# Kernel optimization log

Measured on AMD Instinct MI355X. Metric: run time of the kernel, lower is better.

The kernel has to match this reference:

```python
import jax, jax.numpy as jnp
import numpy as np
from jax import lax

# ---- constants matching init kwargs / proposal_creator(mode='testing') ----
RATIOS = (0.5, 1.0, 2.0)
SCALES = (8.0, 16.0, 32.0)
BASE = 16.0          # generate_anchor_base base_size
STRIDE = 16          # feat_stride
NMS_THRESH = 0.7
N_PRE = 3000         # n_test_pre_nms
N_POST = 300         # n_test_post_nms
MIN_SIZE = 16.0      # min_size * scale (scale=1)


def _anchor_base():
    # (9, 4) xyxy anchors centered at (BASE/2, BASE/2); ratios outer, scales inner
    r = np.array(RATIOS, np.float32)
    s = np.array(SCALES, np.float32)
    hs = (BASE * s[None, :] * np.sqrt(r)[:, None]).reshape(-1)
    ws = (BASE * s[None, :] * np.sqrt(1.0 / r)[:, None]).reshape(-1)
    cx = cy = BASE / 2.0
    return np.stack([cx - ws / 2, cy - hs / 2, cx + ws / 2, cy + hs / 2], 1).astype(np.float32)


def _all_anchors(h, w):
    # _enumerate_shifted_anchor: shift grid flattened y-outer/x-inner to match
    # permute(0,2,3,1).view(n,-1,4) layout of the conv outputs.
    base = jnp.asarray(_anchor_base())                     # (9,4)
    sx = jnp.arange(w, dtype=jnp.float32) * STRIDE
    sy = jnp.arange(h, dtype=jnp.float32) * STRIDE
    SX, SY = jnp.meshgrid(sx, sy)                          # (h,w)
    shifts = jnp.stack([SX, SY, SX, SY], -1).reshape(-1, 4)  # (h*w,4)
    return (shifts[:, None, :] + base[None, :, :]).reshape(-1, 4)  # (h*w*9,4)


def _proposals(loc, score, anchor, img_h, img_w):
    # loc: (K,4) deltas, score: (K,) fg prob, anchor: (K,4) xyxy
    aw = anchor[:, 2] - anchor[:, 0]
    ah = anchor[:, 3] - anchor[:, 1]
    acx = anchor[:, 0] + 0.5 * aw
    acy = anchor[:, 1] + 0.5 * ah
    cx = loc[:, 0] * aw + acx
    cy = loc[:, 1] * ah + acy
    bw = aw * jnp.exp(loc[:, 2])
    bh = ah * jnp.exp(loc[:, 3])
    x1 = jnp.clip(cx - 0.5 * bw, 0.0, img_w)
    y1 = jnp.clip(cy - 0.5 * bh, 0.0, img_h)
    x2 = jnp.clip(cx + 0.5 * bw, 0.0, img_w)
    y2 = jnp.clip(cy + 0.5 * bh, 0.0, img_h)
    boxes = jnp.stack([x1, y1, x2, y2], 1)
    valid = ((x2 - x1) >= MIN_SIZE) & ((y2 - y1) >= MIN_SIZE)
    # min-size filter -> sink invalid boxes with -inf score, then top-k pre-NMS
    masked = jnp.where(valid, score, -jnp.inf)
    _, idx = lax.top_k(masked, N_PRE)
    b = boxes[idx]                                         # (N_PRE,4), score-sorted desc
    v = valid[idx]
    # pairwise IoU (torchvision convention: no +1)
    area = (b[:, 2] - b[:, 0]) * (b[:, 3] - b[:, 1])
    ix1 = jnp.maximum(b[:, None, 0], b[None, :, 0])
    iy1 = jnp.maximum(b[:, None, 1], b[None, :, 1])
    ix2 = jnp.minimum(b[:, None, 2], b[None, :, 2])
    iy2 = jnp.minimum(b[:, None, 3], b[None, :, 3])
    inter = jnp.clip(ix2 - ix1, 0.0) * jnp.clip(iy2 - iy1, 0.0)
    union = area[:, None] + area[None, :] - inter
    iou = jnp.where(union > 0.0, inter / union, 0.0)
    sup = iou > NMS_THRESH                                 # (N_PRE,N_PRE) bool
    # greedy sequential NMS over score order
    ar = jnp.arange(N_PRE)
    def body(keep, i):
        keep = keep & ~(keep[i] & sup[i] & (ar > i))
        return keep, None
    keep, _ = lax.scan(body, v, ar)
    # first N_POST kept boxes (score order); pad by cycling kept boxes
    order = jnp.argsort(jnp.where(keep, ar, N_PRE))        # kept indices first, sorted
    nk = jnp.maximum(keep.sum(), 1)
    pos = jnp.arange(N_POST)
    sel = order[jnp.where(pos < nk, pos, pos % nk)]
    return b[sel]                                          # (N_POST,4)


def setup_inputs() -> dict:
    key = jax.random.key(0)
    ks = jax.random.split(key, 4)
    n, c, h, w = 4, 512, 38, 38
    return {
        "x": jax.random.normal(ks[0], (n, c, h, w), jnp.float32),
        "conv1_w": jax.random.normal(ks[1], (512, 512, 3, 3), jnp.float32) * 0.01,
        "conv1_b": jnp.zeros((512,), jnp.float32),
        "score_w": jax.random.normal(ks[2], (18, 512), jnp.float32) * 0.01,
        "score_b": jnp.zeros((18,), jnp.float32),
        "loc_w": jax.random.normal(ks[3], (36, 512), jnp.float32) * 0.01,
        "loc_b": jnp.zeros((36,), jnp.float32),
        "img_h": 608,
        "img_w": 608,
    }


def reference(x, conv1_w, conv1_b, score_w, score_b, loc_w, loc_b, img_h, img_w):
    n, _, h, w = x.shape
    feat = jax.nn.relu(
        lax.conv_general_dilated(x, conv1_w, (1, 1), "SAME",
                                 dimension_numbers=("NCHW", "OIHW", "NCHW"))
        + conv1_b[None, :, None, None])
    locs = jnp.einsum("nchw,oc->nohw", feat, loc_w) + loc_b[None, :, None, None]
    scores = jnp.einsum("nchw,oc->nohw", feat, score_w) + score_b[None, :, None, None]
    rpn_locs = locs.transpose(0, 2, 3, 1).reshape(n, -1, 4)      # (n, h*w*9, 4)
    rpn_scores = scores.transpose(0, 2, 3, 1).reshape(n, -1, 2)  # (n, h*w*9, 2)
    fg = jax.nn.softmax(rpn_scores, axis=-1)[..., 1]             # (n, h*w*9)
    anchor = _all_anchors(h, w)
    ih = jnp.float32(img_h)
    iw = jnp.float32(img_w)
    rois = jax.vmap(lambda l, s: _proposals(l, s, anchor, ih, iw))(rpn_locs, fg)
    rois_indices = jnp.broadcast_to(
        jnp.arange(n, dtype=x.dtype)[:, None], (n, N_POST))
    return rpn_locs, rpn_scores, rois.reshape(-1, 4), rois_indices, anchor[None]
```

## Files before the change

kernel.cpp:

```cpp
#include <hip/hip_runtime.h>
#include <cstdint>
#include <cstddef>

#define HW    1444
#define NA    12996
#define NPRE  3000
#define NW    47
#define NPOST 300

#define OFF_LOCS   0
#define OFF_SCORES 207936
#define OFF_ROIS   311904
#define OFF_IDX    316704
#define OFF_ANCH   317904

#define INVALID_KEY 0xFFF0000000000000ULL

typedef float f32x2 __attribute__((ext_vector_type(2)));
typedef float f32x4 __attribute__((ext_vector_type(4)));

__device__ inline double as_dim(int raw) {
  if (raw > 0 && raw < 1000000) return (double)raw;
  return (double)__int_as_float(raw);
}

__global__ __launch_bounds__(256) void wt_k(const float* __restrict__ lw,
                                            const float* __restrict__ sw,
                                            float* __restrict__ Wt,
                                            unsigned long long* __restrict__ keys) {
  int t = blockIdx.x * 256 + threadIdx.x;
  if (t < 4 * (16384 - NA)) {
    int n2 = t / (16384 - NA), r = t - n2 * (16384 - NA);
    keys[((size_t)n2 << 14) + NA + r] = ~0ULL;
  }
  if (t >= 64 * 512) return;
  int o = t & 63, c = t >> 6;
  float v = 0.f;
  if (o < 36)      v = lw[o * 512 + c];
  else if (o < 54) v = sw[(o - 36) * 512 + c];
  Wt[t] = v;
}

__global__ __launch_bounds__(256) void conv_k(const float* __restrict__ X,
                                              const float* __restrict__ W,
                                              const float* __restrict__ B,
                                              float* __restrict__ F) {
  __shared__ float Xs[1008];
  __shared__ float Wsf[2304];
  const int tid  = threadIdx.x;
  const int lane = tid & 63;
  const int wv   = tid >> 6;
  const int seg  = wv * 10;
  const int y  = blockIdx.x;
  const int o0 = blockIdx.y * 64;
  const int n  = blockIdx.z;
  const float* xn = X + ((size_t)n * 512) * HW;

  int xsrcA[2]; bool xvalA[2]; bool xactA1;
  {
    int e = tid;
    int cl = e / 120, rem = e - cl * 120, row = rem / 40, colA = rem - row * 40;
    int m = colA - 1, iy = y - 1 + row;
    xvalA[0] = (m >= 0 && m < 38 && iy >= 0 && iy < 38);
    xsrcA[0] = xvalA[0] ? (cl * HW + iy * 38 + m) : 0;
  }
  {
    int e = tid + 256; xactA1 = (e < 480);
    int cl = e / 120, rem = e - cl * 120, row = rem / 40, colA = rem - row * 40;
    int m = colA - 1, iy = y - 1 + row;
    xvalA[1] = xactA1 && (m >= 0 && m < 38 && iy >= 0 && iy < 38);
    xsrcA[1] = xvalA[1] ? (cl * HW + iy * 38 + m) : 0;
  }
  int xsrcB[3]; bool xvalB[3]; bool xactB2;
#pragma unroll
  for (int u = 0; u < 3; ++u) {
    int e = tid + u * 256;
    bool act = (e < 528);
    int cl = e / 132, rem = e - cl * 132, row = rem / 44, colB = rem - row * 44;
    int m = colB - 3, iy = y - 1 + row;
    xvalB[u] = act && (m >= 0 && m < 38 && iy >= 0 && iy < 38);
    xsrcB[u] = xvalB[u] ? (cl * HW + iy * 38 + m) : 0;
    if (u == 2) xactB2 = act;
  }
  int wsrc[9];
#pragma unroll
  for (int u = 0; u < 9; ++u) {
    int e = tid + u * 256;
    int ol = e / 36, t36 = e - ol * 36;
    wsrc[u] = (o0 + ol) * 4608 + t36;
  }

  float xrA[2], xrB[3], wr_[9];
#pragma unroll
  for (int u = 0; u < 2; ++u) xrA[u] = xvalA[u] ? xn[xsrcA[u]] : 0.f;
#pragma unroll
  for (int u = 0; u < 3; ++u) xrB[u] = xvalB[u] ? xn[xsrcB[u]] : 0.f;
#pragma unroll
  for (int u = 0; u < 9; ++u) wr_[u] = W[wsrc[u]];

  double acc[10];
#pragma unroll
  for (int p = 0; p < 10; ++p) acc[p] = 0.;
  f32x2 pA[5], pB[5];
  float pc0 = 0.f;

  const int  xb0   = (wv & 1) ? (480 + seg + 2) : seg;
  const int  cstep = (wv & 1) ? 132 : 120;
  const int  kstep = (wv & 1) ? 44 : 40;

#define WQ_ELEM(t) ((t & 3) == 0 ? wq[(t) >> 2].x : (t & 3) == 1 ? wq[(t) >> 2].y : \
                    (t & 3) == 2 ? wq[(t) >> 2].z : wq[(t) >> 2].w)

  for (int cc = 0; cc < 128; ++cc) {
    __syncthreads();
    Xs[tid] = xrA[0];
    if (xactA1) Xs[tid + 256] = xrA[1];
    Xs[480 + tid] = xrB[0];
    Xs[480 + tid + 256] = xrB[1];
    if (xactB2) Xs[480 + tid + 512] = xrB[2];
#pragma unroll
    for (int u = 0; u < 9; ++u) Wsf[tid + u * 256] = wr_[u];
    __syncthreads();
    if (cc < 127) {
      const int cb = (cc + 1) * 4;
#pragma unroll
      for (int u = 0; u < 2; ++u) xrA[u] = xvalA[u] ? xn[cb * HW + xsrcA[u]] : 0.f;
#pragma unroll
      for (int u = 0; u < 3; ++u) xrB[u] = xvalB[u] ? xn[cb * HW + xsrcB[u]] : 0.f;
#pragma unroll
      for (int u = 0; u < 9; ++u) wr_[u] = W[wsrc[u] + (cc + 1) * 36];
    }
    f32x4 wq[9];
    {
      const f32x4* wrow = (const f32x4*)&Wsf[lane * 36];
#pragma unroll
      for (int q = 0; q < 9; ++q) wq[q] = wrow[q];
    }
    if ((cc & 1) == 0) {
#pragma unroll
      for (int a = 0; a < 5; ++a) { pA[a] = (f32x2)(0.f); pB[a] = (f32x2)(0.f); }
      pc0 = 0.f;
    }
#pragma unroll
    for (int cl = 0; cl < 4; ++cl) {
      f32x2 wp[9];
#pragma unroll
      for (int k = 0; k < 9; ++k) {
        float wv0 = WQ_ELEM(cl * 9 + k);
        wp[k][0] = wv0; wp[k][1] = wv0;
      }
#pragma unroll
      for (int ky = 0; ky < 3; ++ky) {
        const float* xrow = &Xs[xb0 + cl * cstep + ky * kstep];
        f32x4 q0 = *(const f32x4*)(xrow);
        f32x4 q1 = *(const f32x4*)(xrow + 4);
        f32x4 q2 = *(const f32x4*)(xrow + 8);
        f32x2 xp[6];
        xp[0] = __builtin_shufflevector(q0, q0, 0, 1);
        xp[1] = __builtin_shufflevector(q0, q0, 2, 3);
        xp[2] = __builtin_shufflevector(q1, q1, 0, 1);
        xp[3] = __builtin_shufflevector(q1, q1, 2, 3);
        xp[4] = __builtin_shufflevector(q2, q2, 0, 1);
        xp[5] = __builtin_shufflevector(q2, q2, 2, 3);
#pragma unroll
        for (int a = 0; a < 5; ++a)
          asm("v_pk_fma_f32 %0, %1, %2, %0"
              : "+v"(pA[a]) : "v"(xp[a]), "v"(wp[ky * 3 + 0]));
        pc0 = fmaf(wp[ky * 3 + 1][0], xp[0][1], pc0);
#pragma unroll
        for (int a = 0; a < 5; ++a)
          asm("v_pk_fma_f32 %0, %1, %2, %0"
              : "+v"(pB[a]) : "v"(xp[a + 1]), "v"(wp[ky * 3 + 1]));
#pragma unroll
        for (int a = 0; a < 5; ++a)
          asm("v_pk_fma_f32 %0, %1, %2, %0"
              : "+v"(pA[a]) : "v"(xp[a + 1]), "v"(wp[ky * 3 + 2]));
      }
    }
    if (cc & 1) {
      acc[0] += (double)(pA[0][0] + pc0);
#pragma unroll
      for (int p = 1; p < 10; ++p) {
        float sa = pA[p >> 1][p & 1];
        float sb = (p & 1) ? pB[(p - 1) >> 1][0] : pB[(p - 2) >> 1][1];
        acc[p] += (double)(sa + sb);
      }
    }
  }
  double bb = (double)B[o0 + lane];
  float* fp = F + ((size_t)(n * 512 + o0 + lane)) * HW + y * 38;
#pragma unroll
  for (int p = 0; p < 10; ++p) {
    int col = seg + p;
    if (col < 38) fp[col] = (float)fmax(acc[p] + bb, 0.0);
  }
}

__global__ __launch_bounds__(256) void heads_k(const float* __restrict__ F,
                                               const float* __restrict__ Wt,
                                               const float* __restrict__ lb,
                                               const float* __restrict__ sb,
                                               const int* __restrict__ ihp,
                                               const int* __restrict__ iwp,
                                               float* __restrict__ out,
                                               double* __restrict__ boxes,
                                               unsigned long long* __restrict__ keys) {
  __shared__ float sf[512 * 4];
  __shared__ double ssc[4][18];
  __shared__ float sloc[4][36];
  int n = blockIdx.y;
  int p0 = blockIdx.x * 4;
  int tid = threadIdx.x;
  const float* fn = F + ((size_t)n * 512) * HW;
  for (int e = tid; e < 2048; e += 256) {
    int c = e >> 2, pl = e & 3;
    sf[e] = fn[c * HW + p0 + pl];
  }
  __syncthreads();
  int pl = tid & 3, o = tid >> 2;
  double acc = 0.;
  if (o < 54) {
    for (int c = 0; c < 512; ++c)
      acc = fma((double)Wt[(c << 6) | o], (double)sf[(c << 2) | pl], acc);
  }
  int p = p0 + pl;
  if (o < 36) {
    acc += (double)lb[o];
    float v = (float)acc;
    out[OFF_LOCS + ((size_t)n * NA + (size_t)p * 9 + (o >> 2)) * 4 + (o & 3)] = v;
    sloc[pl][o] = v;
  } else if (o < 54) {
    int oo = o - 36;
    acc += (double)sb[oo];
    out[OFF_SCORES + ((size_t)n * NA + (size_t)p * 9 + (oo >> 1)) * 2 + (oo & 1)] = (float)acc;
    ssc[pl][oo] = acc;
  }
  __syncthreads();
  if (tid < 36) {
    int pl2 = tid / 9, a = tid - pl2 * 9;
    double s0 = ssc[pl2][a * 2], s1 = ssc[pl2][a * 2 + 1];
    double mx = fmax(s0, s1);
    double e0 = exp(s0 - mx), e1 = exp(s1 - mx);
    double sc = e1 / (e0 + e1);
    int pp = p0 + pl2;
    int i = pp * 9 + a;
    int ri = a / 3, si = a - ri * 3;
    double sr  = (ri == 0) ? 0.7071067811865476 : (ri == 1 ? 1.0 : 1.4142135623730951);
    double sri = (ri == 0) ? 1.4142135623730951 : (ri == 1 ? 1.0 : 0.7071067811865476);
    double hs = (double)(128 << si) * sr;
    double wd = (double)(128 << si) * sri;
    int py = pp / 38, px = pp - py * 38;
    float sx = (float)(px * 16), sy = (float)(py * 16);
    float fx1 = (float)(8.0 - 0.5 * wd), fy1 = (float)(8.0 - 0.5 * hs);
    float fx2 = (float)(8.0 + 0.5 * wd), fy2 = (float)(8.0 + 0.5 * hs);
    float ax1f = sx + fx1, ay1f = sy + fy1, ax2f = sx + fx2, ay2f = sy + fy2;
    if (n == 0) {
      float* ap = out + OFF_ANCH + (size_t)i * 4;
      ap[0] = ax1f; ap[1] = ay1f; ap[2] = ax2f; ap[3] = ay2f;
    }
    double ax1 = ax1f, ay1 = ay1f, ax2 = ax2f, ay2 = ay2f;
    double aw = ax2 - ax1, ah = ay2 - ay1;
    double acx = ax1 + 0.5 * aw, acy = ay1 + 0.5 * ah;
    double l0 = (double)sloc[pl2][a * 4 + 0], l1 = (double)sloc[pl2][a * 4 + 1];
    double l2 = (double)sloc[pl2][a * 4 + 2], l3 = (double)sloc[pl2][a * 4 + 3];
    double cx = l0 * aw + acx, cy = l1 * ah + acy;
    double bw = aw * exp(l2), bh = ah * exp(l3);
    double iwf = as_dim(iwp[0]), ihf = as_dim(ihp[0]);
    double x1 = fmin(fmax(cx - 0.5 * bw, 0.0), iwf);
    double y1 = fmin(fmax(cy - 0.5 * bh, 0.0), ihf);
    double x2 = fmin(fmax(cx + 0.5 * bw, 0.0), iwf);
    double y2 = fmin(fmax(cy + 0.5 * bh, 0.0), ihf);
    bool valid = ((x2 - x1) >= 16.0) && ((y2 - y1) >= 16.0);
    double* bp = boxes + ((size_t)n * NA + i) * 4;
    bp[0] = x1; bp[1] = y1; bp[2] = x2; bp[3] = y2;
    unsigned long long u = (unsigned long long)__double_as_longlong(sc);
    u = (u >> 63) ? ~u : (u | 0x8000000000000000ULL);
    unsigned long long inv = ~u;
    if (!valid) inv = INVALID_KEY;
    keys[((size_t)n << 14) + i] = (inv & ~0x3FFFULL) | (unsigned long long)i;
  }
}

__global__ __launch_bounds__(1024) void sortA_k(unsigned long long* __restrict__ keys) {
  __shared__ unsigned long long s[8192];
  const int half = blockIdx.x & 1;
  unsigned long long* g = keys + (((size_t)(blockIdx.x >> 1)) << 14) + ((size_t)half << 13);
  const int tid = threadIdx.x;
  for (int i = tid; i < 8192; i += 1024) s[i] = g[i];
  for (int size = 2; size <= 8192; size <<= 1) {
    for (int stride = size >> 1; stride > 0; stride >>= 1) {
      __syncthreads();
      for (int u = tid; u < 4096; u += 1024) {
        int lo = u & (stride - 1);
        int i1 = ((u - lo) << 1) | lo;
        int i2 = i1 + stride;
        bool up = (i1 & size) == 0;
        if (half) up = !up;
        unsigned long long a = s[i1], b = s[i2];
        if ((a > b) == up) { s[i1] = b; s[i2] = a; }
      }
    }
  }
  __syncthreads();
  for (int i = tid; i < 8192; i += 1024) g[i] = s[i];
}

__global__ __launch_bounds__(1024) void sortCG_k(const unsigned long long* __restrict__ keys,
                                                 const double* __restrict__ boxes,
                                                 double* __restrict__ bsort,
                                                 unsigned long long* __restrict__ vw) {
  __shared__ unsigned long long s[8192];
  const int n = blockIdx.x;
  const unsigned long long* g = keys + ((size_t)n << 14);
  const int tid = threadIdx.x;
  for (int i = tid; i < 8192; i += 1024) {
    unsigned long long a = g[i], b = g[i + 8192];
    s[i] = a < b ? a : b;
  }
  for (int stride = 4096; stride > 0; stride >>= 1) {
    __syncthreads();
    for (int u = tid; u < 4096; u += 1024) {
      int lo = u & (stride - 1);
      int i1 = ((u - lo) << 1) | lo;
      int i2 = i1 + stride;
      unsigned long long a = s[i1], b = s[i2];
      if (a > b) { s[i1] = b; s[i2] = a; }
    }
  }
  __syncthreads();
  const int lane = tid & 63;
#pragma unroll
  for (int r3 = 0; r3 < 3; ++r3) {
    int r = r3 * 1024 + tid;
    bool valid = false;
    if (r < NPRE) {
      unsigned long long kk = s[r];
      valid = kk < INVALID_KEY;
      unsigned idx = (unsigned)(kk & 0x3FFFULL);
      const double* bp = boxes + ((size_t)n * NA + idx) * 4;
      double* dp = bsort + ((size_t)n * NPRE + r) * 4;
      dp[0] = bp[0]; dp[1] = bp[1]; dp[2] = bp[2]; dp[3] = bp[3];
    }
    unsigned long long mask = __ballot(valid);
    int w = r >> 6;
    if (lane == 0 && w < NW) vw[n * NW + w] = mask;
  }
}

__global__ __launch_bounds__(256) void iou_k(const double* __restrict__ bsort,
                                             unsigned long long* __restrict__ sup) {
  int t = blockIdx.x * 256 + threadIdx.x;
  if (t >= 4 * NPRE * NW) return;
  int w = t % NW; int rest = t / NW; int i = rest % NPRE; int n = rest / NPRE;
  const double* bb = bsort + (size_t)n * NPRE * 4;
  double bix1 = bb[(size_t)i*4], biy1 = bb[(size_t)i*4+1];
  double bix2 = bb[(size_t)i*4+2], biy2 = bb[(size_t)i*4+3];
  double ai = (bix2 - bix1) * (biy2 - biy1);
  unsigned long long word = 0ULL;
  int j0 = w << 6;
  if (j0 + 63 > i) {
    int lmax = NPRE - j0; if (lmax > 64) lmax = 64;
    for (int l = 0; l < lmax; ++l) {
      int j = j0 + l;
      if (j <= i) continue;
      const double* bj = bb + (size_t)j * 4;
      double aj = (bj[2] - bj[0]) * (bj[3] - bj[1]);
      double xx1 = fmax(bix1, bj[0]), yy1 = fmax(biy1, bj[1]);
      double xx2 = fmin(bix2, bj[2]), yy2 = fmin(biy2, bj[3]);
      double inter = fmax(xx2 - xx1, 0.0) * fmax(yy2 - yy1, 0.0);
      double uni = ai + aj - inter;
      bool supb = (uni > 0.0) && (inter > 0.7 * uni);
      word |= (unsigned long long)supb << l;
    }
  }
  sup[((size_t)n * NPRE + i) * NW + w] = word;
}

__global__ void nms_k(const unsigned long long* __restrict__ sup,
                      const unsigned long long* __restrict__ vwp,
                      const double* __restrict__ bsort,
                      float* __restrict__ out) {
  int n = blockIdx.x; int l = threadIdx.x;
  unsigned long long vw = (l < NW) ? vwp[n * NW + l] : 0ULL;
  unsigned long long remv = 0ULL, keepw = 0ULL;
  const unsigned long long* sbase = sup + (size_t)n * NPRE * NW;
  unsigned long long r = (l < NPRE) ? sbase[(size_t)l * NW] : 0ULL;
  for (int b = 0; b < NW; ++b) {
    unsigned long long rn = 0ULL;
    if (b + 1 < NW) {
      int gi = (b + 1) * 64 + l;
      if (gi < NPRE) rn = sbase[(size_t)gi * NW + (b + 1)];
    }
    unsigned long long kept = __shfl(vw & ~remv, b);
    unsigned long long todo = kept;
    while (todo) {
      int i = __builtin_ctzll(todo);
      unsigned long long ri = __shfl(r, i);
      kept &= ~ri;
      todo &= todo - 1;
      todo &= ~ri;
    }
    if (l == b) keepw = kept;
    unsigned long long m = kept;
    while (m) {
      int i0 = __builtin_ctzll(m); m &= m - 1;
      int i1 = -1, i2 = -1, i3 = -1, i4 = -1, i5 = -1, i6 = -1, i7 = -1;
      if (m) { i1 = __builtin_ctzll(m); m &= m - 1; }
      if (m) { i2 = __builtin_ctzll(m); m &= m - 1; }
      if (m) { i3 = __builtin_ctzll(m); m &= m - 1; }
      if (m) { i4 = __builtin_ctzll(m); m &= m - 1; }
      if (m) { i5 = __builtin_ctzll(m); m &= m - 1; }
      if (m) { i6 = __builtin_ctzll(m); m &= m - 1; }
      if (m) { i7 = __builtin_ctzll(m); m &= m - 1; }
      if (l < NW) {
        const unsigned long long* rb = sbase + (size_t)(b << 6) * NW + l;
        unsigned long long a0 = rb[(size_t)i0 * NW];
        unsigned long long a1 = (i1 >= 0) ? rb[(size_t)i1 * NW] : 0ULL;
        unsigned long long a2 = (i2 >= 0) ? rb[(size_t)i2 * NW] : 0ULL;
        unsigned long long a3 = (i3 >= 0) ? rb[(size_t)i3 * NW] : 0ULL;
        unsigned long long a4 = (i4 >= 0) ? rb[(size_t)i4 * NW] : 0ULL;
        unsigned long long a5 = (i5 >= 0) ? rb[(size_t)i5 * NW] : 0ULL;
        unsigned long long a6 = (i6 >= 0) ? rb[(size_t)i6 * NW] : 0ULL;
        unsigned long long a7 = (i7 >= 0) ? rb[(size_t)i7 * NW] : 0ULL;
        remv |= (((a0 | a1) | (a2 | a3)) | ((a4 | a5) | (a6 | a7)));
      }
    }
    r = rn;
  }
  unsigned long long keep = keepw;
  int cnt = __popcll(keep);
  int pre = cnt;
#pragma unroll
  for (int d = 1; d < 64; d <<= 1) {
    int tt = __shfl_up(pre, d);
    if (l >= d) pre += tt;
  }
  int nk = __shfl(pre, 63);
  int excl = pre - cnt;
  __shared__ float sbox[NPOST * 4];
  unsigned long long m2 = keep; int rank = excl;
  while (m2) {
    int b = __builtin_ctzll(m2);
    m2 &= m2 - 1;
    if (rank < NPOST) {
      int j = (l << 6) + b;
      const double* bj = bsort + ((size_t)n * NPRE + j) * 4;
      sbox[rank*4]   = (float)bj[0]; sbox[rank*4+1] = (float)bj[1];
      sbox[rank*4+2] = (float)bj[2]; sbox[rank*4+3] = (float)bj[3];
    }
    ++rank;
  }
  __syncthreads();
  if (nk == 0 && l == 0) {
    const double* b0 = bsort + (size_t)n * NPRE * 4;
    sbox[0] = (float)b0[0]; sbox[1] = (float)b0[1];
    sbox[2] = (float)b0[2]; sbox[3] = (float)b0[3];
  }
  __syncthreads();
  int nke = nk > 0 ? nk : 1;
  for (int r2 = l; r2 < NPOST; r2 += 64) {
    int src = r2 < nke ? r2 : r2 % nke;
    float4 b4 = *(float4*)(sbox + src * 4);
    *(float4*)(out + OFF_ROIS + ((size_t)n * NPOST + r2) * 4) = b4;
    out[OFF_IDX + n * NPOST + r2] = (float)n;
  }
}

extern "C" void kernel_launch(void* const* d_in, const int* in_sizes, int n_in,
                              void* d_out, int out_size, void* d_ws, size_t ws_size,
                              hipStream_t stream) {
  const float* X  = (const float*)d_in[0];
  const float* CW = (const float*)d_in[1];
  const float* CB = (const float*)d_in[2];
  const float* SW = (const float*)d_in[3];
  const float* SB = (const float*)d_in[4];
  const float* LW = (const float*)d_in[5];
  const float* LB = (const float*)d_in[6];
  const int*   IH = (const int*)d_in[7];
  const int*   IW = (const int*)d_in[8];
  float* out = (float*)d_out;
  char* ws = (char*)d_ws;

  float* feat = (float*)(ws + 0);
  unsigned long long* sup  = (unsigned long long*)(ws + 0);
  float* Wt    = (float*)(ws + 11829248);
  double* boxes= (double*)(ws + 12376192);
  unsigned long long* keys = (unsigned long long*)(ws + 14039680);
  double* bsort= (double*)(ws + 14563968);
  unsigned long long* vw   = (unsigned long long*)(ws + 14947968);

  hipLaunchKernelGGL(wt_k,    dim3(128),      dim3(256),  0, stream, LW, SW, Wt, keys);
  hipLaunchKernelGGL(conv_k,  dim3(38, 8, 4), dim3(256),  0, stream, X, CW, CB, feat);
  hipLaunchKernelGGL(heads_k, dim3(361, 4),   dim3(256),  0, stream,
                     feat, Wt, LB, SB, IH, IW, out, boxes, keys);
  hipLaunchKernelGGL(sortA_k, dim3(8),        dim3(1024), 0, stream, keys);
  hipLaunchKernelGGL(sortCG_k,dim3(4),        dim3(1024), 0, stream, keys, boxes, bsort, vw);
  hipLaunchKernelGGL(iou_k,   dim3((4*NPRE*NW + 255) / 256), dim3(256), 0, stream, bsort, sup);
  hipLaunchKernelGGL(nms_k,   dim3(4),        dim3(64),   0, stream, sup, vw, bsort, out);
}
```

Before: 968.6 us.

## Split bitonic sort across more blocks and tile IoU mask per 64-row block

The first bitonic stages (sizes up to 2048) now run as 32 independent blocks instead of 8, with direction chosen from the global index, and only the final merge stages stay in the 8-block kernel. The IoU kernel is restructured so that each block handles 64 rows of one image: lanes map to rows and waves stride over column words, so a wavefront reads the same column box together (a broadcast load). Results are staged in LDS and written out coalesced. This trades some redundant work in skipped-lower-triangle words for better memory access and more parallelism in the sort.

```diff
diff --git a/kernel.cpp b/kernel.cpp
--- a/kernel.cpp
+++ b/kernel.cpp
@@ -281,13 +281,39 @@
   }
 }
 
-__global__ __launch_bounds__(1024) void sortA_k(unsigned long long* __restrict__ keys) {
+__global__ __launch_bounds__(1024) void sortA1_k(unsigned long long* __restrict__ keys) {
+  __shared__ unsigned long long s[2048];
+  const int c = blockIdx.x;
+  const int batch = c >> 3, chunk = c & 7;
+  unsigned long long* g = keys + ((size_t)batch << 14) + ((size_t)chunk << 11);
+  const int tid = threadIdx.x;
+  for (int i = tid; i < 2048; i += 1024) s[i] = g[i];
+  const int gbase = chunk << 11;
+  const bool hflip = (chunk >= 4);
+  for (int size = 2; size <= 2048; size <<= 1) {
+    for (int stride = size >> 1; stride > 0; stride >>= 1) {
+      __syncthreads();
+      int u = tid;
+      int lo = u & (stride - 1);
+      int i1 = ((u - lo) << 1) | lo;
+      int i2 = i1 + stride;
+      bool up = (((gbase + i1) & size) == 0);
+      if (hflip) up = !up;
+      unsigned long long a = s[i1], b = s[i2];
+      if ((a > b) == up) { s[i1] = b; s[i2] = a; }
+    }
+  }
+  __syncthreads();
+  for (int i = tid; i < 2048; i += 1024) g[i] = s[i];
+}
+
+__global__ __launch_bounds__(1024) void sortA2_k(unsigned long long* __restrict__ keys) {
   __shared__ unsigned long long s[8192];
   const int half = blockIdx.x & 1;
   unsigned long long* g = keys + (((size_t)(blockIdx.x >> 1)) << 14) + ((size_t)half << 13);
   const int tid = threadIdx.x;
   for (int i = tid; i < 8192; i += 1024) s[i] = g[i];
-  for (int size = 2; size <= 8192; size <<= 1) {
+  for (int size = 4096; size <= 8192; size <<= 1) {
     for (int stride = size >> 1; stride > 0; stride >>= 1) {
       __syncthreads();
       for (int u = tid; u < 4096; u += 1024) {
@@ -349,31 +375,47 @@
 
 __global__ __launch_bounds__(256) void iou_k(const double* __restrict__ bsort,
                                              unsigned long long* __restrict__ sup) {
-  int t = blockIdx.x * 256 + threadIdx.x;
-  if (t >= 4 * NPRE * NW) return;
-  int w = t % NW; int rest = t / NW; int i = rest % NPRE; int n = rest / NPRE;
+  __shared__ unsigned long long tile[64 * 49];
+  const int ib = blockIdx.x;
+  const int n  = blockIdx.y;
+  const int tid = threadIdx.x;
+  const int lane = tid & 63;
+  const int wv = tid >> 6;
+  const int i0 = ib * 64;
+  const int i  = i0 + lane;
+  const int iclamp = i < NPRE ? i : NPRE - 1;
   const double* bb = bsort + (size_t)n * NPRE * 4;
-  double bix1 = bb[(size_t)i*4], biy1 = bb[(size_t)i*4+1];
-  double bix2 = bb[(size_t)i*4+2], biy2 = bb[(size_t)i*4+3];
+  double bix1 = bb[(size_t)iclamp * 4 + 0], biy1 = bb[(size_t)iclamp * 4 + 1];
+  double bix2 = bb[(size_t)iclamp * 4 + 2], biy2 = bb[(size_t)iclamp * 4 + 3];
   double ai = (bix2 - bix1) * (biy2 - biy1);
-  unsigned long long word = 0ULL;
-  int j0 = w << 6;
-  if (j0 + 63 > i) {
-    int lmax = NPRE - j0; if (lmax > 64) lmax = 64;
-    for (int l = 0; l < lmax; ++l) {
-      int j = j0 + l;
-      if (j <= i) continue;
-      const double* bj = bb + (size_t)j * 4;
-      double aj = (bj[2] - bj[0]) * (bj[3] - bj[1]);
-      double xx1 = fmax(bix1, bj[0]), yy1 = fmax(biy1, bj[1]);
-      double xx2 = fmin(bix2, bj[2]), yy2 = fmin(biy2, bj[3]);
-      double inter = fmax(xx2 - xx1, 0.0) * fmax(yy2 - yy1, 0.0);
-      double uni = ai + aj - inter;
-      bool supb = (uni > 0.0) && (inter > 0.7 * uni);
-      word |= (unsigned long long)supb << l;
-    }
-  }
-  sup[((size_t)n * NPRE + i) * NW + w] = word;
+  for (int w = wv; w < NW; w += 4) {
+    int j0 = w << 6;
+    unsigned long long word = 0ULL;
+    if (j0 + 63 > i0) {
+      int lmax = NPRE - j0; if (lmax > 64) lmax = 64;
+      for (int l2 = 0; l2 < lmax; ++l2) {
+        int j = j0 + l2;
+        const double* bj = bb + (size_t)j * 4;
+        double bjx1 = bj[0], bjy1 = bj[1], bjx2 = bj[2], bjy2 = bj[3];
+        double aj = (bjx2 - bjx1) * (bjy2 - bjy1);
+        double xx1 = fmax(bix1, bjx1), yy1 = fmax(biy1, bjy1);
+        double xx2 = fmin(bix2, bjx2), yy2 = fmin(biy2, bjy2);
+        double inter = fmax(xx2 - xx1, 0.0) * fmax(yy2 - yy1, 0.0);
+        double uni = ai + aj - inter;
+        bool supb = (j > i) && (uni > 0.0) && (inter > 0.7 * uni);
+        word |= (unsigned long long)supb << l2;
+      }
+    }
+    tile[lane * 49 + w] = word;
+  }
+  __syncthreads();
+  int rows = NPRE - i0; if (rows > 64) rows = 64;
+  int total = rows * NW;
+  unsigned long long* gout = sup + ((size_t)n * NPRE + i0) * NW;
+  for (int idx = tid; idx < total; idx += 256) {
+    int il = idx / NW, w = idx - il * NW;
+    gout[idx] = tile[il * 49 + w];
+  }
 }
 
 __global__ void nms_k(const unsigned long long* __restrict__ sup,
@@ -489,12 +531,13 @@
   double* bsort= (double*)(ws + 14563968);
   unsigned long long* vw   = (unsigned long long*)(ws + 14947968);
 
-  hipLaunchKernelGGL(wt_k,    dim3(128),      dim3(256),  0, stream, LW, SW, Wt, keys);
-  hipLaunchKernelGGL(conv_k,  dim3(38, 8, 4), dim3(256),  0, stream, X, CW, CB, feat);
-  hipLaunchKernelGGL(heads_k, dim3(361, 4),   dim3(256),  0, stream,
+  hipLaunchKernelGGL(wt_k,     dim3(128),      dim3(256),  0, stream, LW, SW, Wt, keys);
+  hipLaunchKernelGGL(conv_k,   dim3(38, 8, 4), dim3(256),  0, stream, X, CW, CB, feat);
+  hipLaunchKernelGGL(heads_k,  dim3(361, 4),   dim3(256),  0, stream,
                      feat, Wt, LB, SB, IH, IW, out, boxes, keys);
-  hipLaunchKernelGGL(sortA_k, dim3(8),        dim3(1024), 0, stream, keys);
-  hipLaunchKernelGGL(sortCG_k,dim3(4),        dim3(1024), 0, stream, keys, boxes, bsort, vw);
-  hipLaunchKernelGGL(iou_k,   dim3((4*NPRE*NW + 255) / 256), dim3(256), 0, stream, bsort, sup);
-  hipLaunchKernelGGL(nms_k,   dim3(4),        dim3(64),   0, stream, sup, vw, bsort, out);
-}
+  hipLaunchKernelGGL(sortA1_k, dim3(32),       dim3(1024), 0, stream, keys);
+  hipLaunchKernelGGL(sortA2_k, dim3(8),        dim3(1024), 0, stream, keys);
+  hipLaunchKernelGGL(sortCG_k, dim3(4),        dim3(1024), 0, stream, keys, boxes, bsort, vw);
+  hipLaunchKernelGGL(iou_k,    dim3(47, 4),    dim3(256),  0, stream, bsort, sup);
+  hipLaunchKernelGGL(nms_k,    dim3(4),        dim3(64),   0, stream, sup, vw, bsort, out);
+}
```

After: 1.000 ms. 1.03x slower.
